# Optimization experiments

Hardware: AMD Instinct MI355X
Metric: run time of the kernel (lower is better)

## Reference

```python
import jax, jax.numpy as jnp
import numpy as np

EPS = 1e-5
B, L, DM, DI, DR, DS, K = 1, 1024, 2048, 4096, 128, 16, 3
DT_MAX, DT_MIN, DT_FLOOR = 0.1, 0.001, 1e-4


def setup_inputs() -> dict:
    key = jax.random.key(0)
    ks = jax.random.split(key, 10)
    sc = lambda k, sh, s=0.02: (jax.random.normal(k, sh, jnp.float32) * s)
    # dt_proj bias init (softplus-inverse of dt sampled log-uniform in [dt_min, dt_max])
    dt = jnp.exp(jax.random.uniform(ks[7], (DI,), jnp.float32)
                 * (np.log(DT_MAX) - np.log(DT_MIN)) + np.log(DT_MIN))
    dt = jnp.clip(dt, DT_FLOOR, None)
    inv_dt = dt + jnp.log(-jnp.expm1(-dt))
    dt_std = DR ** (-0.5)  # dt_rank**-0.5 * dt_scale
    return {
        "x": jax.random.normal(ks[0], (B, L, DM), jnp.float32),
        "h": jnp.zeros((B, L, DI, DS), jnp.float32),
        "norm_w": jnp.ones((DM,), jnp.float32),
        "in_proj_w": sc(ks[1], (2 * DI, DM)),
        "conv_w": sc(ks[2], (DI, 1, K), 0.1),      # depthwise: (out=DI, in/groups=1, K)
        "conv_b": jnp.zeros((DI,), jnp.float32),
        "x_proj_w": sc(ks[3], (DR + 2 * DS, DI)),
        "dt_proj_w": jax.random.uniform(ks[4], (DI, DR), jnp.float32, -dt_std, dt_std),
        "dt_proj_b": inv_dt,
        "A_log": jnp.log(jnp.tile(jnp.arange(1, DS + 1, dtype=jnp.float32), (DI, 1))),
        "D": jnp.ones((DI,), jnp.float32),
        "out_proj_w": sc(ks[5], (DM, DI)),
    }


def reference(x, h, norm_w, in_proj_w, conv_w, conv_b, x_proj_w,
              dt_proj_w, dt_proj_b, A_log, D, out_proj_w):
    # RMSNorm
    xn = x * jax.lax.rsqrt(jnp.mean(x * x, axis=-1, keepdims=True) + EPS) * norm_w
    # in_proj -> split into x-branch and gate z
    xz = xn @ in_proj_w.T                      # (B,L,2*DI)
    xs, z = xz[..., :DI], xz[..., DI:]
    # depthwise conv over sequence (padding preserves L for odd K)
    xc = jax.lax.conv_general_dilated(
        jnp.transpose(xs, (0, 2, 1)), conv_w, (1,), [((K - 1) // 2, (K - 1) // 2)],
        dimension_numbers=("NCH", "OIH", "NCH"), feature_group_count=DI)
    xc = jnp.transpose(xc, (0, 2, 1)) + conv_b  # (B,L,DI)
    xc = jax.nn.silu(xc)
    # ssm_step (elementwise over L; h is per-position state)
    A = -jnp.exp(A_log)                        # (DI,DS)
    dBC = xc @ x_proj_w.T                      # (B,L,DR+2*DS)
    delta = jax.nn.softplus(dBC[..., :DR] @ dt_proj_w.T + dt_proj_b)  # (B,L,DI)
    Bm = dBC[..., DR:DR + DS]                  # (B,L,DS)
    Cm = dBC[..., DR + DS:]                    # (B,L,DS)
    deltaA = jnp.exp(delta[..., None] * A)     # (B,L,DI,DS)
    BX = delta[..., None] * Bm[:, :, None, :] * xc[..., None]  # (B,L,DI,DS)
    h_new = deltaA * h + BX                    # (B,L,DI,DS)
    y = jnp.einsum("blds,bls->bld", h_new, Cm) + D * xc
    out = (y * jax.nn.silu(z)) @ out_proj_w.T + xn  # residual adds normed x
    return out, h_new
```

## Files before the change

### kernel.cpp

```cpp
#include <hip/hip_runtime.h>
#include <hip/hip_bf16.h>
#include <math.h>

#define L_   1024
#define DM_  2048
#define DI_  4096
#define DR_  128
#define DS_  16
#define DBC_ 160

typedef __attribute__((ext_vector_type(4))) float f32x4;
typedef __attribute__((ext_vector_type(8))) short s16x8;

__device__ inline unsigned short f2b(float f) {
  unsigned int u = __float_as_uint(f);
  u += 0x7fffu + ((u >> 16) & 1u);
  return (unsigned short)(u >> 16);
}
__device__ inline float b2f(unsigned short u) {
  return __uint_as_float(((unsigned int)u) << 16);
}

__device__ inline void gload_lds16(const void* g, void* l) {
  __builtin_amdgcn_global_load_lds(
      (const __attribute__((address_space(1))) void*)g,
      (__attribute__((address_space(3))) void*)l, 16, 0, 0);
}

__launch_bounds__(256)
__global__ void rmsnorm_kernel(const float* __restrict__ x, const float* __restrict__ w,
                               float* __restrict__ xn, unsigned short* __restrict__ xnb) {
  int l = blockIdx.x;
  const float4* xr = (const float4*)(x + (size_t)l * DM_);
  const float4* wr = (const float4*)w;
  float4 v0 = xr[threadIdx.x];
  float4 v1 = xr[threadIdx.x + 256];
  float ss = v0.x*v0.x + v0.y*v0.y + v0.z*v0.z + v0.w*v0.w
           + v1.x*v1.x + v1.y*v1.y + v1.z*v1.z + v1.w*v1.w;
  for (int off = 32; off > 0; off >>= 1) ss += __shfl_down(ss, off, 64);
  __shared__ float sbuf[4];
  int lane = threadIdx.x & 63, wid = threadIdx.x >> 6;
  if (lane == 0) sbuf[wid] = ss;
  __syncthreads();
  float tot = sbuf[0] + sbuf[1] + sbuf[2] + sbuf[3];
  float scale = rsqrtf(tot / (float)DM_ + 1e-5f);
  float4 w0 = wr[threadIdx.x], w1 = wr[threadIdx.x + 256];
  float4 o0, o1;
  o0.x = v0.x * scale * w0.x; o0.y = v0.y * scale * w0.y;
  o0.z = v0.z * scale * w0.z; o0.w = v0.w * scale * w0.w;
  o1.x = v1.x * scale * w1.x; o1.y = v1.y * scale * w1.y;
  o1.z = v1.z * scale * w1.z; o1.w = v1.w * scale * w1.w;
  float4* outr = (float4*)(xn + (size_t)l * DM_);
  outr[threadIdx.x] = o0;
  outr[threadIdx.x + 256] = o1;
  uint2 p0, p1;
  p0.x = (unsigned)f2b(o0.x) | ((unsigned)f2b(o0.y) << 16);
  p0.y = (unsigned)f2b(o0.z) | ((unsigned)f2b(o0.w) << 16);
  p1.x = (unsigned)f2b(o1.x) | ((unsigned)f2b(o1.y) << 16);
  p1.y = (unsigned)f2b(o1.z) | ((unsigned)f2b(o1.w) << 16);
  uint2* ob = (uint2*)(xnb + (size_t)l * DM_);
  ob[threadIdx.x] = p0;
  ob[threadIdx.x + 256] = p1;
}

__launch_bounds__(256)
__global__ void convert_weights_kernel(const float* __restrict__ w_in, const float* __restrict__ w_out,
                                       const float* __restrict__ w_dt, const float* __restrict__ w_xp,
                                       unsigned short* __restrict__ wib, unsigned short* __restrict__ wob,
                                       unsigned short* __restrict__ dtwb, unsigned short* __restrict__ xpwb) {
  const int N1 = 2 * DI_ * DM_ / 4;
  const int N2 = DM_ * DI_ / 4;
  const int N3 = DI_ * DR_ / 4;
  const int N4 = DBC_ * DI_ / 4;
  int i = blockIdx.x * 256 + threadIdx.x;
  const float* src; unsigned short* dst; int off;
  if (i < N1)                { src = w_in;  dst = wib;  off = i; }
  else if (i < N1 + N2)      { src = w_out; dst = wob;  off = i - N1; }
  else if (i < N1 + N2 + N3) { src = w_dt;  dst = dtwb; off = i - N1 - N2; }
  else if (i < N1 + N2 + N3 + N4) { src = w_xp; dst = xpwb; off = i - N1 - N2 - N3; }
  else return;
  float4 v = ((const float4*)src)[off];
  uint2 p;
  p.x = (unsigned)f2b(v.x) | ((unsigned)f2b(v.y) << 16);
  p.y = (unsigned)f2b(v.z) | ((unsigned)f2b(v.w) << 16);
  ((uint2*)dst)[off] = p;
}

template<int EPI>
__launch_bounds__(256)
__global__ void gemm_bf16_mfma(const unsigned short* __restrict__ A,
                               const unsigned short* __restrict__ W,
                               float* __restrict__ C, int M, int N, int K,
                               const float* __restrict__ aux) {
  __shared__ unsigned short As[128 * 32];
  __shared__ unsigned short Ws[128 * 32];
  int bm = blockIdx.y * 128, bn = blockIdx.x * 128;
  int tid = threadIdx.x;
  int w = tid >> 6, lane = tid & 63;
  int wr = (w >> 1) * 64, wc = (w & 1) * 64;
  f32x4 acc[4][4];
#pragma unroll
  for (int m = 0; m < 4; m++)
#pragma unroll
    for (int n = 0; n < 4; n++) acc[m][n] = (f32x4){0.f, 0.f, 0.f, 0.f};

  int kb = lane >> 4, r = lane & 15;
  for (int k0 = 0; k0 < K; k0 += 32) {
#pragma unroll
    for (int i = 0; i < 2; i++) {
      int ch = (i * 4 + w) * 64 + lane;
      int row = ch >> 2, kc = ch & 3;
      gload_lds16(A + (size_t)(bm + row) * K + k0 + kc * 8, As + ch * 8);
      gload_lds16(W + (size_t)(bn + row) * K + k0 + kc * 8, Ws + ch * 8);
    }
    asm volatile("s_waitcnt vmcnt(0)" ::: "memory");
    __syncthreads();
    s16x8 a[4], b[4];
#pragma unroll
    for (int m = 0; m < 4; m++)
      a[m] = *(const s16x8*)(As + (wr + m * 16 + r) * 32 + kb * 8);
#pragma unroll
    for (int n = 0; n < 4; n++)
      b[n] = *(const s16x8*)(Ws + (wc + n * 16 + r) * 32 + kb * 8);
#pragma unroll
    for (int m = 0; m < 4; m++)
#pragma unroll
      for (int n = 0; n < 4; n++)
        acc[m][n] = __builtin_amdgcn_mfma_f32_16x16x32_bf16(a[m], b[n], acc[m][n], 0, 0, 0);
    __syncthreads();
  }
  int q = lane >> 4;
#pragma unroll
  for (int m = 0; m < 4; m++) {
#pragma unroll
    for (int n = 0; n < 4; n++) {
#pragma unroll
      for (int j = 0; j < 4; j++) {
        int row = bm + wr + m * 16 + q * 4 + j;
        int col = bn + wc + n * 16 + r;
        float v = acc[m][n][j];
        if (EPI == 1) {
          v += aux[col];
          v = fmaxf(v, 0.f) + log1pf(__expf(-fabsf(v)));
        }
        if (EPI == 2) v += aux[(size_t)row * N + col];
        C[(size_t)row * N + col] = v;
      }
    }
  }
}

template<int EPI>
__launch_bounds__(256)
__global__ void gemm_bf16_mfma_bm64(const unsigned short* __restrict__ A,
                                    const unsigned short* __restrict__ W,
                                    float* __restrict__ C, int M, int N, int K,
                                    const float* __restrict__ aux) {
  __shared__ unsigned short As[64 * 32];
  __shared__ unsigned short Ws[128 * 32];
  int bm = blockIdx.y * 64, bn = blockIdx.x * 128;
  int tid = threadIdx.x;
  int w = tid >> 6, lane = tid & 63;
  int wr = (w >> 1) * 32, wc = (w & 1) * 64;
  f32x4 acc[2][4];
#pragma unroll
  for (int m = 0; m < 2; m++)
#pragma unroll
    for (int n = 0; n < 4; n++) acc[m][n] = (f32x4){0.f, 0.f, 0.f, 0.f};

  int kb = lane >> 4, r = lane & 15;
  for (int k0 = 0; k0 < K; k0 += 32) {
    {
      int ch = w * 64 + lane;
      int row = ch >> 2, kc = ch & 3;
      gload_lds16(A + (size_t)(bm + row) * K + k0 + kc * 8, As + ch * 8);
    }
#pragma unroll
    for (int i = 0; i < 2; i++) {
      int ch = (i * 4 + w) * 64 + lane;
      int row = ch >> 2, kc = ch & 3;
      gload_lds16(W + (size_t)(bn + row) * K + k0 + kc * 8, Ws + ch * 8);
    }
    asm volatile("s_waitcnt vmcnt(0)" ::: "memory");
    __syncthreads();
    s16x8 a[2], b[4];
#pragma unroll
    for (int m = 0; m < 2; m++)
      a[m] = *(const s16x8*)(As + (wr + m * 16 + r) * 32 + kb * 8);
#pragma unroll
    for (int n = 0; n < 4; n++)
      b[n] = *(const s16x8*)(Ws + (wc + n * 16 + r) * 32 + kb * 8);
#pragma unroll
    for (int m = 0; m < 2; m++)
#pragma unroll
      for (int n = 0; n < 4; n++)
        acc[m][n] = __builtin_amdgcn_mfma_f32_16x16x32_bf16(a[m], b[n], acc[m][n], 0, 0, 0);
    __syncthreads();
  }
  int q = lane >> 4;
#pragma unroll
  for (int m = 0; m < 2; m++) {
#pragma unroll
    for (int n = 0; n < 4; n++) {
#pragma unroll
      for (int j = 0; j < 4; j++) {
        int row = bm + wr + m * 16 + q * 4 + j;
        int col = bn + wc + n * 16 + r;
        float v = acc[m][n][j];
        if (EPI == 2) v += aux[(size_t)row * N + col];
        C[(size_t)row * N + col] = v;
      }
    }
  }
}

__launch_bounds__(256)
__global__ void conv_silu_kernel(const float* __restrict__ xz, const float* __restrict__ cw,
                                 const float* __restrict__ cb, unsigned short* __restrict__ xcb) {
  int idx = blockIdx.x * 256 + threadIdx.x;
  int l = idx >> 12, d = idx & (DI_ - 1);
  float w0 = cw[d * 3 + 0], w1 = cw[d * 3 + 1], w2 = cw[d * 3 + 2];
  float acc = cb[d];
  const float* base = xz + d;
  if (l > 0)      acc = fmaf(w0, base[(size_t)(l - 1) * (2 * DI_)], acc);
  acc = fmaf(w1, base[(size_t)l * (2 * DI_)], acc);
  if (l < L_ - 1) acc = fmaf(w2, base[(size_t)(l + 1) * (2 * DI_)], acc);
  float sig = 1.f / (1.f + __expf(-acc));
  xcb[idx] = f2b(acc * sig);
}

__launch_bounds__(256)
__global__ void xproj_stage1_mfma(const unsigned short* __restrict__ xcb,
                                  const unsigned short* __restrict__ Wb,
                                  float* __restrict__ part) {
  __shared__ unsigned short As[64 * 32];
  __shared__ unsigned short Bs[160 * 32];
  int sp = blockIdx.x;
  int l0 = blockIdx.y * 64;
  int tid = threadIdx.x, w = tid >> 6, lane = tid & 63;
  int wr = (w >> 1) * 32, wc = (w & 1) * 80;
  int kb = lane >> 4, r = lane & 15;
  f32x4 acc[2][5];
#pragma unroll
  for (int m = 0; m < 2; m++)
#pragma unroll
    for (int n = 0; n < 5; n++) acc[m][n] = (f32x4){0.f, 0.f, 0.f, 0.f};

  for (int kt = 0; kt < 8; kt++) {
    int k0 = sp * 256 + kt * 32;
    {
      int ch = w * 64 + lane;
      int row = ch >> 2, kc = ch & 3;
      gload_lds16(xcb + (size_t)(l0 + row) * DI_ + k0 + kc * 8, As + ch * 8);
    }
#pragma unroll
    for (int i = 0; i < 3; i++) {
      int g = i * 4 + w;
      if (g < 10) {
        int ch = g * 64 + lane;
        int row = ch >> 2, kc = ch & 3;
        gload_lds16(Wb + (size_t)row * DI_ + k0 + kc * 8, Bs + ch * 8);
      }
    }
    asm volatile("s_waitcnt vmcnt(0)" ::: "memory");
    __syncthreads();
    s16x8 a[2], b[5];
#pragma unroll
    for (int m = 0; m < 2; m++)
      a[m] = *(const s16x8*)(As + (wr + m * 16 + r) * 32 + kb * 8);
#pragma unroll
    for (int n = 0; n < 5; n++)
      b[n] = *(const s16x8*)(Bs + (wc + n * 16 + r) * 32 + kb * 8);
#pragma unroll
    for (int m = 0; m < 2; m++)
#pragma unroll
      for (int n = 0; n < 5; n++)
        acc[m][n] = __builtin_amdgcn_mfma_f32_16x16x32_bf16(a[m], b[n], acc[m][n], 0, 0, 0);
    __syncthreads();
  }
  int q = lane >> 4;
  float* pb = part + (size_t)sp * (L_ * DBC_) + (size_t)l0 * DBC_;
#pragma unroll
  for (int m = 0; m < 2; m++)
#pragma unroll
    for (int n = 0; n < 5; n++)
#pragma unroll
      for (int j = 0; j < 4; j++)
        pb[(size_t)(wr + m * 16 + q * 4 + j) * DBC_ + wc + n * 16 + r] = acc[m][n][j];
}

__launch_bounds__(256)
__global__ void xproj_stage2(const float* __restrict__ part, float* __restrict__ dBC,
                             unsigned short* __restrict__ dtb) {
  int i = blockIdx.x * 256 + threadIdx.x;
  float s = 0.f;
#pragma unroll
  for (int sp = 0; sp < 16; sp++) s += part[(size_t)sp * (L_ * DBC_) + i];
  dBC[i] = s;
  int l = i / DBC_, col = i - l * DBC_;
  if (col < DR_) dtb[(size_t)l * DR_ + col] = f2b(s);
}

__launch_bounds__(256)
__global__ void ssm_kernel2(const float* __restrict__ xz, const unsigned short* __restrict__ xcb,
                            const float* __restrict__ dBC, const float* __restrict__ delta,
                            const float* __restrict__ h, const float* __restrict__ A_log,
                            const float* __restrict__ Dp, float* __restrict__ h_out,
                            unsigned short* __restrict__ yzb) {
  int pair = threadIdx.x >> 2;
  int q = threadIdx.x & 3;
  for (int base = blockIdx.x * 64; base < L_ * DI_; base += gridDim.x * 64) {
    int idx = base + pair;
    int l = idx >> 12, d = idx & (DI_ - 1);
    float dv = delta[idx];
    float xv = b2f(xcb[idx]);
    float4 hv = *(const float4*)(h + (size_t)idx * DS_ + q * 4);
    float4 Al = *(const float4*)(A_log + (size_t)d * DS_ + q * 4);
    float4 Bv = *(const float4*)(dBC + (size_t)l * DBC_ + DR_ + q * 4);
    float4 Cv = *(const float4*)(dBC + (size_t)l * DBC_ + DR_ + DS_ + q * 4);
    float4 hn;
    hn.x = __expf(dv * -__expf(Al.x)) * hv.x + dv * Bv.x * xv;
    hn.y = __expf(dv * -__expf(Al.y)) * hv.y + dv * Bv.y * xv;
    hn.z = __expf(dv * -__expf(Al.z)) * hv.z + dv * Bv.z * xv;
    hn.w = __expf(dv * -__expf(Al.w)) * hv.w + dv * Bv.w * xv;
    *(float4*)(h_out + (size_t)idx * DS_ + q * 4) = hn;
    float y = hn.x * Cv.x + hn.y * Cv.y + hn.z * Cv.z + hn.w * Cv.w;
    y += __shfl_xor(y, 1, 64);
    y += __shfl_xor(y, 2, 64);
    if (q == 0) {
      y = fmaf(Dp[d], xv, y);
      float zv = xz[(size_t)l * (2 * DI_) + DI_ + d];
      float sig = 1.f / (1.f + __expf(-zv));
      yzb[idx] = f2b(y * zv * sig);
    }
  }
}

extern "C" void kernel_launch(void* const* d_in, const int* in_sizes, int n_in,
                              void* d_out, int out_size, void* d_ws, size_t ws_size,
                              hipStream_t stream) {
  const float* x         = (const float*)d_in[0];
  const float* h         = (const float*)d_in[1];
  const float* norm_w    = (const float*)d_in[2];
  const float* in_proj_w = (const float*)d_in[3];
  const float* conv_w    = (const float*)d_in[4];
  const float* conv_b    = (const float*)d_in[5];
  const float* x_proj_w  = (const float*)d_in[6];
  const float* dt_proj_w = (const float*)d_in[7];
  const float* dt_proj_b = (const float*)d_in[8];
  const float* A_log     = (const float*)d_in[9];
  const float* Dvec      = (const float*)d_in[10];
  const float* out_projw = (const float*)d_in[11];

  float* out   = (float*)d_out;
  float* h_out = out + (size_t)L_ * DM_;

  float* ws    = (float*)d_ws;
  float* xn    = ws;
  float* xz    = xn    + (size_t)L_ * DM_;
  float* dBC   = xz    + (size_t)L_ * 2 * DI_;
  float* delta = dBC   + (size_t)L_ * DBC_;
  float* part  = delta + (size_t)L_ * DI_;
  unsigned short* xnb  = (unsigned short*)(part + (size_t)16 * L_ * DBC_);
  unsigned short* wib  = xnb  + (size_t)L_ * DM_;
  unsigned short* wob  = wib  + (size_t)2 * DI_ * DM_;
  unsigned short* yzb  = wob  + (size_t)DM_ * DI_;
  unsigned short* dtb  = yzb  + (size_t)L_ * DI_;
  unsigned short* dtwb = dtb  + (size_t)L_ * DR_;
  unsigned short* xpwb = dtwb + (size_t)DI_ * DR_;
  unsigned short* xcb  = xpwb + (size_t)DBC_ * DI_;

  rmsnorm_kernel<<<L_, 256, 0, stream>>>(x, norm_w, xn, xnb);
  convert_weights_kernel<<<(2 * DI_ * DM_ + DM_ * DI_ + DI_ * DR_ + DBC_ * DI_) / 4 / 256, 256, 0, stream>>>(
      in_proj_w, out_projw, dt_proj_w, x_proj_w, wib, wob, dtwb, xpwb);
  gemm_bf16_mfma<0><<<dim3(2 * DI_ / 128, L_ / 128), 256, 0, stream>>>(
      xnb, wib, xz, L_, 2 * DI_, DM_, nullptr);
  conv_silu_kernel<<<L_ * DI_ / 256, 256, 0, stream>>>(xz, conv_w, conv_b, xcb);
  xproj_stage1_mfma<<<dim3(16, 16), 256, 0, stream>>>(xcb, xpwb, part);
  xproj_stage2<<<L_ * DBC_ / 256, 256, 0, stream>>>(part, dBC, dtb);
  gemm_bf16_mfma<1><<<dim3(DI_ / 128, L_ / 128), 256, 0, stream>>>(
      dtb, dtwb, delta, L_, DI_, DR_, dt_proj_b);
  ssm_kernel2<<<4096, 256, 0, stream>>>(
      xz, xcb, dBC, delta, h, A_log, Dvec, h_out, yzb);
  gemm_bf16_mfma_bm64<2><<<dim3(DM_ / 128, L_ / 64), 256, 0, stream>>>(
      yzb, wob, out, L_, DM_, DI_, xn);
}
```

Baseline: 341.0 us.

## Store xz and delta intermediates as bf16, merge rmsnorm with weight conversion, swizzle GEMM blocks

The in_proj and dt_proj GEMMs now write their outputs as bf16, and the conv, SSM and output stages read those bf16 buffers. This halves intermediate memory traffic at the cost of precision on z, xs and delta. The RMSNorm and weight-conversion kernels are merged into one launch to remove a kernel boundary. Both GEMMs remap block indices with an XCD-style swizzle to improve L2 locality across chiplets.

```diff
diff --git a/kernel.cpp b/kernel.cpp
--- a/kernel.cpp
+++ b/kernel.cpp
@@ -28,51 +28,51 @@
 }
 
 __launch_bounds__(256)
-__global__ void rmsnorm_kernel(const float* __restrict__ x, const float* __restrict__ w,
-                               float* __restrict__ xn, unsigned short* __restrict__ xnb) {
-  int l = blockIdx.x;
-  const float4* xr = (const float4*)(x + (size_t)l * DM_);
-  const float4* wr = (const float4*)w;
-  float4 v0 = xr[threadIdx.x];
-  float4 v1 = xr[threadIdx.x + 256];
-  float ss = v0.x*v0.x + v0.y*v0.y + v0.z*v0.z + v0.w*v0.w
-           + v1.x*v1.x + v1.y*v1.y + v1.z*v1.z + v1.w*v1.w;
-  for (int off = 32; off > 0; off >>= 1) ss += __shfl_down(ss, off, 64);
-  __shared__ float sbuf[4];
-  int lane = threadIdx.x & 63, wid = threadIdx.x >> 6;
-  if (lane == 0) sbuf[wid] = ss;
-  __syncthreads();
-  float tot = sbuf[0] + sbuf[1] + sbuf[2] + sbuf[3];
-  float scale = rsqrtf(tot / (float)DM_ + 1e-5f);
-  float4 w0 = wr[threadIdx.x], w1 = wr[threadIdx.x + 256];
-  float4 o0, o1;
-  o0.x = v0.x * scale * w0.x; o0.y = v0.y * scale * w0.y;
-  o0.z = v0.z * scale * w0.z; o0.w = v0.w * scale * w0.w;
-  o1.x = v1.x * scale * w1.x; o1.y = v1.y * scale * w1.y;
-  o1.z = v1.z * scale * w1.z; o1.w = v1.w * scale * w1.w;
-  float4* outr = (float4*)(xn + (size_t)l * DM_);
-  outr[threadIdx.x] = o0;
-  outr[threadIdx.x + 256] = o1;
-  uint2 p0, p1;
-  p0.x = (unsigned)f2b(o0.x) | ((unsigned)f2b(o0.y) << 16);
-  p0.y = (unsigned)f2b(o0.z) | ((unsigned)f2b(o0.w) << 16);
-  p1.x = (unsigned)f2b(o1.x) | ((unsigned)f2b(o1.y) << 16);
-  p1.y = (unsigned)f2b(o1.z) | ((unsigned)f2b(o1.w) << 16);
-  uint2* ob = (uint2*)(xnb + (size_t)l * DM_);
-  ob[threadIdx.x] = p0;
-  ob[threadIdx.x + 256] = p1;
-}
-
-__launch_bounds__(256)
-__global__ void convert_weights_kernel(const float* __restrict__ w_in, const float* __restrict__ w_out,
-                                       const float* __restrict__ w_dt, const float* __restrict__ w_xp,
-                                       unsigned short* __restrict__ wib, unsigned short* __restrict__ wob,
-                                       unsigned short* __restrict__ dtwb, unsigned short* __restrict__ xpwb) {
+__global__ void rms_convert_kernel(const float* __restrict__ x, const float* __restrict__ w,
+                                   float* __restrict__ xn, unsigned short* __restrict__ xnb,
+                                   const float* __restrict__ w_in, const float* __restrict__ w_out,
+                                   const float* __restrict__ w_dt, const float* __restrict__ w_xp,
+                                   unsigned short* __restrict__ wib, unsigned short* __restrict__ wob,
+                                   unsigned short* __restrict__ dtwb, unsigned short* __restrict__ xpwb) {
+  if (blockIdx.x < L_) {
+    int l = blockIdx.x;
+    const float4* xr = (const float4*)(x + (size_t)l * DM_);
+    const float4* wr = (const float4*)w;
+    float4 v0 = xr[threadIdx.x];
+    float4 v1 = xr[threadIdx.x + 256];
+    float ss = v0.x*v0.x + v0.y*v0.y + v0.z*v0.z + v0.w*v0.w
+             + v1.x*v1.x + v1.y*v1.y + v1.z*v1.z + v1.w*v1.w;
+    for (int off = 32; off > 0; off >>= 1) ss += __shfl_down(ss, off, 64);
+    __shared__ float sbuf[4];
+    int lane = threadIdx.x & 63, wid = threadIdx.x >> 6;
+    if (lane == 0) sbuf[wid] = ss;
+    __syncthreads();
+    float tot = sbuf[0] + sbuf[1] + sbuf[2] + sbuf[3];
+    float scale = rsqrtf(tot / (float)DM_ + 1e-5f);
+    float4 w0 = wr[threadIdx.x], w1 = wr[threadIdx.x + 256];
+    float4 o0, o1;
+    o0.x = v0.x * scale * w0.x; o0.y = v0.y * scale * w0.y;
+    o0.z = v0.z * scale * w0.z; o0.w = v0.w * scale * w0.w;
+    o1.x = v1.x * scale * w1.x; o1.y = v1.y * scale * w1.y;
+    o1.z = v1.z * scale * w1.z; o1.w = v1.w * scale * w1.w;
+    float4* outr = (float4*)(xn + (size_t)l * DM_);
+    outr[threadIdx.x] = o0;
+    outr[threadIdx.x + 256] = o1;
+    uint2 p0, p1;
+    p0.x = (unsigned)f2b(o0.x) | ((unsigned)f2b(o0.y) << 16);
+    p0.y = (unsigned)f2b(o0.z) | ((unsigned)f2b(o0.w) << 16);
+    p1.x = (unsigned)f2b(o1.x) | ((unsigned)f2b(o1.y) << 16);
+    p1.y = (unsigned)f2b(o1.z) | ((unsigned)f2b(o1.w) << 16);
+    uint2* ob = (uint2*)(xnb + (size_t)l * DM_);
+    ob[threadIdx.x] = p0;
+    ob[threadIdx.x + 256] = p1;
+    return;
+  }
   const int N1 = 2 * DI_ * DM_ / 4;
   const int N2 = DM_ * DI_ / 4;
   const int N3 = DI_ * DR_ / 4;
   const int N4 = DBC_ * DI_ / 4;
-  int i = blockIdx.x * 256 + threadIdx.x;
+  int i = (blockIdx.x - L_) * 256 + threadIdx.x;
   const float* src; unsigned short* dst; int off;
   if (i < N1)                { src = w_in;  dst = wib;  off = i; }
   else if (i < N1 + N2)      { src = w_out; dst = wob;  off = i - N1; }
@@ -90,11 +90,16 @@
 __launch_bounds__(256)
 __global__ void gemm_bf16_mfma(const unsigned short* __restrict__ A,
                                const unsigned short* __restrict__ W,
-                               float* __restrict__ C, int M, int N, int K,
+                               void* __restrict__ Cv_, int M, int N, int K,
                                const float* __restrict__ aux) {
   __shared__ unsigned short As[128 * 32];
   __shared__ unsigned short Ws[128 * 32];
-  int bm = blockIdx.y * 128, bn = blockIdx.x * 128;
+  int nwg = gridDim.x * gridDim.y;
+  int flat = blockIdx.y * gridDim.x + blockIdx.x;
+  int q8 = nwg >> 3;
+  int swz = (flat & 7) * q8 + (flat >> 3);
+  int bxi = swz % gridDim.x, byi = swz / gridDim.x;
+  int bm = byi * 128, bn = bxi * 128;
   int tid = threadIdx.x;
   int w = tid >> 6, lane = tid & 63;
   int wr = (w >> 1) * 64, wc = (w & 1) * 64;
@@ -142,15 +147,16 @@
         if (EPI == 1) {
           v += aux[col];
           v = fmaxf(v, 0.f) + log1pf(__expf(-fabsf(v)));
+          ((unsigned short*)Cv_)[(size_t)row * N + col] = f2b(v);
         }
-        if (EPI == 2) v += aux[(size_t)row * N + col];
-        C[(size_t)row * N + col] = v;
+        if (EPI == 3) {
+          ((unsigned short*)Cv_)[(size_t)row * N + col] = f2b(v);
+        }
       }
     }
   }
 }
 
-template<int EPI>
 __launch_bounds__(256)
 __global__ void gemm_bf16_mfma_bm64(const unsigned short* __restrict__ A,
                                     const unsigned short* __restrict__ W,
@@ -158,7 +164,12 @@
                                     const float* __restrict__ aux) {
   __shared__ unsigned short As[64 * 32];
   __shared__ unsigned short Ws[128 * 32];
-  int bm = blockIdx.y * 64, bn = blockIdx.x * 128;
+  int nwg = gridDim.x * gridDim.y;
+  int flat = blockIdx.y * gridDim.x + blockIdx.x;
+  int q8 = nwg >> 3;
+  int swz = (flat & 7) * q8 + (flat >> 3);
+  int bxi = swz % gridDim.x, byi = swz / gridDim.x;
+  int bm = byi * 64, bn = bxi * 128;
   int tid = threadIdx.x;
   int w = tid >> 6, lane = tid & 63;
   int wr = (w >> 1) * 32, wc = (w & 1) * 64;
@@ -206,25 +217,23 @@
       for (int j = 0; j < 4; j++) {
         int row = bm + wr + m * 16 + q * 4 + j;
         int col = bn + wc + n * 16 + r;
-        float v = acc[m][n][j];
-        if (EPI == 2) v += aux[(size_t)row * N + col];
-        C[(size_t)row * N + col] = v;
+        C[(size_t)row * N + col] = acc[m][n][j] + aux[(size_t)row * N + col];
       }
     }
   }
 }
 
 __launch_bounds__(256)
-__global__ void conv_silu_kernel(const float* __restrict__ xz, const float* __restrict__ cw,
+__global__ void conv_silu_kernel(const unsigned short* __restrict__ xzb, const float* __restrict__ cw,
                                  const float* __restrict__ cb, unsigned short* __restrict__ xcb) {
   int idx = blockIdx.x * 256 + threadIdx.x;
   int l = idx >> 12, d = idx & (DI_ - 1);
   float w0 = cw[d * 3 + 0], w1 = cw[d * 3 + 1], w2 = cw[d * 3 + 2];
   float acc = cb[d];
-  const float* base = xz + d;
-  if (l > 0)      acc = fmaf(w0, base[(size_t)(l - 1) * (2 * DI_)], acc);
-  acc = fmaf(w1, base[(size_t)l * (2 * DI_)], acc);
-  if (l < L_ - 1) acc = fmaf(w2, base[(size_t)(l + 1) * (2 * DI_)], acc);
+  const unsigned short* base = xzb + d;
+  if (l > 0)      acc = fmaf(w0, b2f(base[(size_t)(l - 1) * (2 * DI_)]), acc);
+  acc = fmaf(w1, b2f(base[(size_t)l * (2 * DI_)]), acc);
+  if (l < L_ - 1) acc = fmaf(w2, b2f(base[(size_t)(l + 1) * (2 * DI_)]), acc);
   float sig = 1.f / (1.f + __expf(-acc));
   xcb[idx] = f2b(acc * sig);
 }
@@ -302,8 +311,8 @@
 }
 
 __launch_bounds__(256)
-__global__ void ssm_kernel2(const float* __restrict__ xz, const unsigned short* __restrict__ xcb,
-                            const float* __restrict__ dBC, const float* __restrict__ delta,
+__global__ void ssm_kernel2(const unsigned short* __restrict__ xzb, const unsigned short* __restrict__ xcb,
+                            const float* __restrict__ dBC, const unsigned short* __restrict__ deltab,
                             const float* __restrict__ h, const float* __restrict__ A_log,
                             const float* __restrict__ Dp, float* __restrict__ h_out,
                             unsigned short* __restrict__ yzb) {
@@ -312,7 +321,7 @@
   for (int base = blockIdx.x * 64; base < L_ * DI_; base += gridDim.x * 64) {
     int idx = base + pair;
     int l = idx >> 12, d = idx & (DI_ - 1);
-    float dv = delta[idx];
+    float dv = b2f(deltab[idx]);
     float xv = b2f(xcb[idx]);
     float4 hv = *(const float4*)(h + (size_t)idx * DS_ + q * 4);
     float4 Al = *(const float4*)(A_log + (size_t)d * DS_ + q * 4);
@@ -329,7 +338,7 @@
     y += __shfl_xor(y, 2, 64);
     if (q == 0) {
       y = fmaf(Dp[d], xv, y);
-      float zv = xz[(size_t)l * (2 * DI_) + DI_ + d];
+      float zv = b2f(xzb[(size_t)l * (2 * DI_) + DI_ + d]);
       float sig = 1.f / (1.f + __expf(-zv));
       yzb[idx] = f2b(y * zv * sig);
     }
@@ -357,31 +366,31 @@
 
   float* ws    = (float*)d_ws;
   float* xn    = ws;
-  float* xz    = xn    + (size_t)L_ * DM_;
-  float* dBC   = xz    + (size_t)L_ * 2 * DI_;
-  float* delta = dBC   + (size_t)L_ * DBC_;
-  float* part  = delta + (size_t)L_ * DI_;
-  unsigned short* xnb  = (unsigned short*)(part + (size_t)16 * L_ * DBC_);
-  unsigned short* wib  = xnb  + (size_t)L_ * DM_;
-  unsigned short* wob  = wib  + (size_t)2 * DI_ * DM_;
-  unsigned short* yzb  = wob  + (size_t)DM_ * DI_;
-  unsigned short* dtb  = yzb  + (size_t)L_ * DI_;
-  unsigned short* dtwb = dtb  + (size_t)L_ * DR_;
-  unsigned short* xpwb = dtwb + (size_t)DI_ * DR_;
-  unsigned short* xcb  = xpwb + (size_t)DBC_ * DI_;
-
-  rmsnorm_kernel<<<L_, 256, 0, stream>>>(x, norm_w, xn, xnb);
-  convert_weights_kernel<<<(2 * DI_ * DM_ + DM_ * DI_ + DI_ * DR_ + DBC_ * DI_) / 4 / 256, 256, 0, stream>>>(
-      in_proj_w, out_projw, dt_proj_w, x_proj_w, wib, wob, dtwb, xpwb);
-  gemm_bf16_mfma<0><<<dim3(2 * DI_ / 128, L_ / 128), 256, 0, stream>>>(
-      xnb, wib, xz, L_, 2 * DI_, DM_, nullptr);
-  conv_silu_kernel<<<L_ * DI_ / 256, 256, 0, stream>>>(xz, conv_w, conv_b, xcb);
+  float* dBC   = xn    + (size_t)L_ * DM_;
+  float* part  = dBC   + (size_t)L_ * DBC_;
+  unsigned short* xnb   = (unsigned short*)(part + (size_t)16 * L_ * DBC_);
+  unsigned short* wib   = xnb   + (size_t)L_ * DM_;
+  unsigned short* wob   = wib   + (size_t)2 * DI_ * DM_;
+  unsigned short* yzb   = wob   + (size_t)DM_ * DI_;
+  unsigned short* dtb   = yzb   + (size_t)L_ * DI_;
+  unsigned short* dtwb  = dtb   + (size_t)L_ * DR_;
+  unsigned short* xpwb  = dtwb  + (size_t)DI_ * DR_;
+  unsigned short* xcb   = xpwb  + (size_t)DBC_ * DI_;
+  unsigned short* xzb   = xcb   + (size_t)L_ * DI_;
+  unsigned short* deltab= xzb   + (size_t)L_ * 2 * DI_;
+
+  const int CONV_BLKS = (2 * DI_ * DM_ + DM_ * DI_ + DI_ * DR_ + DBC_ * DI_) / 4 / 256;
+  rms_convert_kernel<<<L_ + CONV_BLKS, 256, 0, stream>>>(
+      x, norm_w, xn, xnb, in_proj_w, out_projw, dt_proj_w, x_proj_w, wib, wob, dtwb, xpwb);
+  gemm_bf16_mfma<3><<<dim3(2 * DI_ / 128, L_ / 128), 256, 0, stream>>>(
+      xnb, wib, xzb, L_, 2 * DI_, DM_, nullptr);
+  conv_silu_kernel<<<L_ * DI_ / 256, 256, 0, stream>>>(xzb, conv_w, conv_b, xcb);
   xproj_stage1_mfma<<<dim3(16, 16), 256, 0, stream>>>(xcb, xpwb, part);
   xproj_stage2<<<L_ * DBC_ / 256, 256, 0, stream>>>(part, dBC, dtb);
   gemm_bf16_mfma<1><<<dim3(DI_ / 128, L_ / 128), 256, 0, stream>>>(
-      dtb, dtwb, delta, L_, DI_, DR_, dt_proj_b);
+      dtb, dtwb, deltab, L_, DI_, DR_, dt_proj_b);
   ssm_kernel2<<<4096, 256, 0, stream>>>(
-      xz, xcb, dBC, delta, h, A_log, Dvec, h_out, yzb);
-  gemm_bf16_mfma_bm64<2><<<dim3(DM_ / 128, L_ / 64), 256, 0, stream>>>(
+      xzb, xcb, dBC, deltab, h, A_log, Dvec, h_out, yzb);
+  gemm_bf16_mfma_bm64<<<dim3(DM_ / 128, L_ / 64), 256, 0, stream>>>(
       yzb, wob, out, L_, DM_, DI_, xn);
 }
```

Result: faster. 330.7 us (-3.0%).
